# Kernel optimization log

Measured on AMD Instinct MI355X. Metric: run time of the kernel, lower is better.

## Reference

```python
import jax, jax.numpy as jnp
import numpy as np

L, D, H, DH, W, G, FF = 2, 768, 12, 64, 256, 64, 3072  # W = one-sided window (attention_window=512)
B, S = 2, 4096
NEG = -1e9


def setup_inputs() -> dict:
    key = jax.random.key(0)
    ks = jax.random.split(key, 16)
    inp = {}
    inp['hidden_states'] = jax.random.normal(ks[0], (B, S, D), jnp.float32)
    # HF Longformer convention: <0 masked, >0 global, 0 local. First G tokens are global.
    inp['attention_mask'] = jnp.zeros((B, S), jnp.float32).at[:, :G].set(1.0)
    inp['padding_len'] = 0
    inp['level_hierarchy'] = 0
    def w(k, shape):
        return (jax.random.normal(k, shape, jnp.float32) * 0.02)
    for i, n in enumerate(['Wq', 'Wk', 'Wv', 'Wqg', 'Wkg', 'Wvg', 'Wo']):
        inp[n] = w(ks[1 + i], (L, D, D))
        inp['b' + n[1:].lower()] = jnp.zeros((L, D), jnp.float32)
    inp['Wi'] = w(ks[8], (L, D, FF)); inp['bi'] = jnp.zeros((L, FF), jnp.float32)
    inp['Wo2'] = w(ks[9], (L, FF, D)); inp['bo2'] = jnp.zeros((L, D), jnp.float32)
    for n in ['ln1', 'ln2']:
        inp[n + '_g'] = jnp.ones((L, D), jnp.float32)
        inp[n + '_b'] = jnp.zeros((L, D), jnp.float32)
    return inp


def _ln(x, g, b):
    mu = jnp.mean(x, -1, keepdims=True)
    var = jnp.mean(jnp.square(x - mu), -1, keepdims=True)
    return (x - mu) * jax.lax.rsqrt(var + 1e-5) * g + b


def _chunk3(x, nc, w):
    # x: [..., S, d] -> [..., nc, 3w, d]: keys of chunks (c-1, c, c+1), zero-padded at the ends
    shp = x.shape
    xr = x.reshape(shp[:-2] + (nc, w, shp[-1]))
    pad = [(0, 0)] * xr.ndim
    pad[-3] = (1, 1)
    xp = jnp.pad(xr, pad)
    return jnp.concatenate([xp[..., :-2, :, :], xp[..., 1:-1, :, :], xp[..., 2:, :, :]], axis=-2)


def _layer(h, mask, Wq, bq, Wk, bk, Wv, bv, Wqg, bqg, Wkg, bkg, Wvg, bvg,
           Wo, bo, ln1_g, ln1_b, Wi, bi, Wo2, bo2, ln2_g, ln2_b):
    Bb, Ss, Dd = h.shape
    nc = Ss // W
    scale = 1.0 / np.sqrt(DH)
    def heads(x):
        return x.reshape(Bb, Ss, H, DH).transpose(0, 2, 1, 3)  # [B,H,S,dh]
    q = heads(h @ Wq + bq) * scale
    k = heads(h @ Wk + bk)
    v = heads(h @ Wv + bv)
    # --- sliding-window (banded) attention, chunked ---
    qc = q.reshape(Bb, H, nc, W, DH)
    k3 = _chunk3(k, nc, W)  # [B,H,nc,3W,dh]
    v3 = _chunk3(v, nc, W)
    local = jnp.einsum('bhcid,bhcjd->bhcij', qc, k3)  # [B,H,nc,W,3W]
    i = jnp.arange(W)[:, None]
    j = jnp.arange(3 * W)[None, :]
    band_ok = jnp.abs(j - W - i) <= W                              # [W,3W]
    keypos = jnp.arange(nc)[:, None, None] * W + (j - W)[None]     # [nc,1,3W]
    in_range = (keypos >= 0) & (keypos < Ss)
    # masked and global keys are removed from the windowed attention (handled via global cols)
    key_local = _chunk3((mask == 0).astype(h.dtype)[..., None], nc, W)[..., 0] > 0.5  # [B,nc,3W]
    valid = band_ok[None, None] & in_range[None] & key_local[:, :, None, :]  # [B,nc,W,3W]
    local = jnp.where(valid[:, None], local, NEG)
    # --- global key columns (every token attends to the G global tokens) ---
    kg, vg = k[:, :, :G], v[:, :, :G]
    sg = jnp.einsum('bhsd,bhgd->bhsg', q, kg).reshape(Bb, H, nc, W, G)
    probs = jax.nn.softmax(jnp.concatenate([sg, local], axis=-1), axis=-1)
    pg, pl = probs[..., :G], probs[..., G:]
    out = (jnp.einsum('bhcig,bhgd->bhcid', pg, vg)
           + jnp.einsum('bhcij,bhcjd->bhcid', pl, v3)).reshape(Bb, H, Ss, DH)
    # --- global token rows: full attention with dedicated global projections ---
    qg = heads(h @ Wqg + bqg)[:, :, :G] * scale
    kgf = heads(h @ Wkg + bkg)
    vgf = heads(h @ Wvg + bvg)
    add = jnp.where(mask < 0, NEG, 0.0)[:, None, None, :]
    pgl = jax.nn.softmax(jnp.einsum('bhgd,bhsd->bhgs', qg, kgf) + add, axis=-1)
    out = out.at[:, :, :G].set(jnp.einsum('bhgs,bhsd->bhgd', pgl, vgf))
    out = jnp.where((mask < 0)[:, None, :, None], 0.0, out)
    attn = out.transpose(0, 2, 1, 3).reshape(Bb, Ss, Dd) @ Wo + bo
    h = _ln(attn + h, ln1_g, ln1_b)
    ff = jax.nn.gelu(h @ Wi + bi, approximate=False) @ Wo2 + bo2
    return _ln(ff + h, ln2_g, ln2_b)


def reference(hidden_states, attention_mask, padding_len, level_hierarchy,
              Wq, bq, Wk, bk, Wv, bv, Wqg, bqg, Wkg, bkg, Wvg, bvg,
              Wo, bo, ln1_g, ln1_b, Wi, bi, Wo2, bo2, ln2_g, ln2_b):
    h = hidden_states
    for l in range(L):
        h = _layer(h, attention_mask,
                   Wq[l], bq[l], Wk[l], bk[l], Wv[l], bv[l],
                   Wqg[l], bqg[l], Wkg[l], bkg[l], Wvg[l], bvg[l],
                   Wo[l], bo[l], ln1_g[l], ln1_b[l],
                   Wi[l], bi[l], Wo2[l], bo2[l], ln2_g[l], ln2_b[l])
    if padding_len > 0:
        h = h[:, :-padding_len]
    return h
```

## Files before the change

### kernel.cpp

```cpp
#include <hip/hip_runtime.h>

#define B_ 2
#define S_ 4096
#define D_ 768
#define H_ 12
#define DH_ 64
#define W_ 256
#define G_ 64
#define FF_ 3072
#define L_ 2
#define M_ (B_*S_)
#define NEGV -1e9f
#define NSPLIT 16

typedef short bf16x8 __attribute__((ext_vector_type(8)));
typedef float f32x4 __attribute__((ext_vector_type(4)));
typedef unsigned short u16;
typedef unsigned short u16x4 __attribute__((ext_vector_type(4)));

__device__ __forceinline__ u16 f2bf(float f) {
  union { float f; unsigned u; } a; a.f = f;
  unsigned r = a.u + 0x7FFFu + ((a.u >> 16) & 1u);
  return (u16)(r >> 16);
}
__device__ __forceinline__ float b2f(u16 u) {
  union { unsigned u; float f; } a; a.u = ((unsigned)u) << 16;
  return a.f;
}

__device__ __forceinline__ f32x4 mfma16(bf16x8 a, bf16x8 b, f32x4 c) {
  return __builtin_amdgcn_mfma_f32_16x16x32_bf16(a, b, c, 0, 0, 0);
}

__device__ __forceinline__ void gload16(const u16* g, u16* l) {
  __builtin_amdgcn_global_load_lds((const __attribute__((address_space(1))) void*)g,
                                   (__attribute__((address_space(3))) void*)l, 16, 0, 0);
}

__device__ __forceinline__ int xcd_swz(int bid, int nwg) {
  if ((nwg & 7) == 0) {
    int cpx = nwg >> 3;
    bid = (bid & 7) * cpx + (bid >> 3);
  }
  return bid;
}

struct Ptr7 { const float* p[7]; };
__global__ __launch_bounds__(256) void wtrans7(Ptr7 in, u16* __restrict__ out) {
  __shared__ float tile[32][33];
  int z = blockIdx.z;
  int slab = z >> 1, l = z & 1;
  const float* src = in.p[slab] + (size_t)l * D_ * D_;
  u16* dst = out + (size_t)z * D_ * D_;
  int k0 = blockIdx.y * 32, n0 = blockIdx.x * 32;
  int tx = threadIdx.x, ty = threadIdx.y;
#pragma unroll
  for (int i = 0; i < 4; i++)
    tile[ty + i*8][tx] = src[(size_t)(k0 + ty + i*8) * D_ + n0 + tx];
  __syncthreads();
#pragma unroll
  for (int i = 0; i < 4; i++)
    dst[(size_t)(n0 + ty + i*8) * D_ + k0 + tx] = f2bf(tile[tx][ty + i*8]);
}

__global__ __launch_bounds__(256) void wtrans(const float* __restrict__ in,
                                              u16* __restrict__ out, int K, int N) {
  __shared__ float tile[32][33];
  size_t base = (size_t)blockIdx.z * K * N;
  int k0 = blockIdx.y * 32, n0 = blockIdx.x * 32;
  int tx = threadIdx.x, ty = threadIdx.y;
#pragma unroll
  for (int i = 0; i < 4; i++)
    tile[ty + i*8][tx] = in[base + (size_t)(k0 + ty + i*8) * N + n0 + tx];
  __syncthreads();
#pragma unroll
  for (int i = 0; i < 4; i++)
    out[base + (size_t)(n0 + ty + i*8) * K + k0 + tx] = f2bf(tile[tx][ty + i*8]);
}

__global__ __launch_bounds__(256) void conv_b(const float* __restrict__ in,
                                              u16* __restrict__ outb, int n4) {
  int i = blockIdx.x * 256 + threadIdx.x;
  if (i >= n4) return;
  float4 v = ((const float4*)in)[i];
  u16x4 o;
  o[0] = f2bf(v.x); o[1] = f2bf(v.y); o[2] = f2bf(v.z); o[3] = f2bf(v.w);
  ((u16x4*)outb)[i] = o;
}

template <int MODE>
__device__ __forceinline__ float epi_post(float v) {
  if (MODE == 2) return v * 0.125f;
  if (MODE == 3) {
    float y = 0.79788456f * (v + 0.044715f * v * v * v);
    float e = __expf(fminf(2.f * y, 20.f));
    return v * e / (e + 1.f);
  }
  return v;
}

struct Bias5 { const float* p[5]; };

#define VMC4() asm volatile("s_waitcnt vmcnt(4)" ::: "memory")
#define VMC0() asm volatile("s_waitcnt vmcnt(0)" ::: "memory")
#define GPH_PRE() do { __builtin_amdgcn_s_barrier(); \
  asm volatile("s_waitcnt lgkmcnt(0)" ::: "memory"); \
  __builtin_amdgcn_sched_barrier(0); } while (0)
#define GPH_PRE_NOLDS() do { __builtin_amdgcn_s_barrier(); \
  __builtin_amdgcn_sched_barrier(0); } while (0)
#define GPH_POST() do { __builtin_amdgcn_sched_barrier(0); \
  __builtin_amdgcn_s_barrier(); } while (0)
#define GPH_MFMA(AF, BF, QM, QN) do { \
  __builtin_amdgcn_s_setprio(1); \
  _Pragma("unroll") for (int mi = 0; mi < 4; mi++) \
  _Pragma("unroll") for (int nj = 0; nj < 2; nj++) \
  _Pragma("unroll") for (int ks = 0; ks < 2; ks++) \
    acc[(QM)*4+mi][(QN)*2+nj] = mfma16(AF[mi][ks], BF[nj][ks], acc[(QM)*4+mi][(QN)*2+nj]); \
  __builtin_amdgcn_s_setprio(0); } while (0)

template <int MODE, int NW>
__global__ __launch_bounds__(512, 2) void gemm256p(const u16* __restrict__ A,
                                                   const u16* __restrict__ Wbase,
                                                   Bias5 bp,
                                                   u16* __restrict__ OutBase,
                                                   int Kdim, int Nstride, int l) {
  __shared__ u16 sh[65536];
  int gx = gridDim.x;
  int bid = blockIdx.x + blockIdx.y * gx;
  bid = xcd_swz(bid, gx * gridDim.y);
  int bxx = bid % gx, by = bid / gx;
  int bm = by * 256;
  int widx, bn;
  const u16* Bt; u16* Cb; const float* bias;
  if (NW == 5) {
    widx = bxx / 3;
    bn = (bxx % 3) * 256;
    int slab = widx + (widx >= 3 ? 1 : 0);
    Bt = Wbase + ((size_t)slab * L_ + l) * (size_t)D_ * D_;
    Cb = OutBase + (size_t)slab * M_ * D_;
    bias = bp.p[widx];
  } else {
    widx = 0;
    bn = bxx * 256;
    Bt = Wbase; Cb = OutBase; bias = bp.p[0];
  }
  int tid = threadIdx.x;
  int lane = tid & 63, wid = tid >> 6;
  int wr = wid >> 2, wc = wid & 3;
  int lr = lane & 15, lg = lane >> 4;

  int rr0 = tid >> 3, slot0 = tid & 7;
  int c80 = slot0 ^ (rr0 & 7);
  const u16* pA = A + (size_t)(bm + rr0) * Kdim + c80 * 8;
  const u16* pB = Bt + (size_t)(bn + rr0) * Kdim + c80 * 8;

  auto stA = [&](int buf, int h, int kt) {
    u16* base = sh + buf * 16384;
    gload16(pA + (size_t)(h * 128) * Kdim + kt * 64, &base[(h * 1024 + tid) * 8]);
    gload16(pA + (size_t)(h * 128 + 64) * Kdim + kt * 64, &base[(h * 1024 + 512 + tid) * 8]);
  };
  auto stB = [&](int buf, int h, int kt) {
    u16* base = sh + 32768 + buf * 16384;
    gload16(pB + (size_t)(h * 128) * Kdim + kt * 64, &base[(h * 1024 + tid) * 8]);
    gload16(pB + (size_t)(h * 128 + 64) * Kdim + kt * 64, &base[(h * 1024 + 512 + tid) * 8]);
  };
  auto ldA = [&](bf16x8 (&af)[4][2], int c, int qm) {
    const u16* base = sh + c * 16384;
#pragma unroll
    for (int mi = 0; mi < 4; mi++)
#pragma unroll
      for (int ks = 0; ks < 2; ks++) {
        int row = wr * 128 + qm * 64 + mi * 16 + lr;
        int c8 = ks * 4 + lg;
        af[mi][ks] = *(const bf16x8*)&base[(row * 8 + (c8 ^ (row & 7))) * 8];
      }
  };
  auto ldB = [&](bf16x8 (&bf)[2][2], int c, int qn) {
    const u16* base = sh + 32768 + c * 16384;
#pragma unroll
    for (int nj = 0; nj < 2; nj++)
#pragma unroll
      for (int ks = 0; ks < 2; ks++) {
        int row = wc * 64 + qn * 32 + nj * 16 + lr;
        int c8 = ks * 4 + lg;
        bf[nj][ks] = *(const bf16x8*)&base[(row * 8 + (c8 ^ (row & 7))) * 8];
      }
  };

  f32x4 acc[8][4] = {};
  int nt = Kdim >> 6;

  stA(0, 0, 0); stA(0, 1, 0);
  stB(0, 0, 0); stB(0, 1, 0);
  stB(1, 0, 1); stB(1, 1, 1);
  VMC4();
  __builtin_amdgcn_s_barrier();

  bf16x8 af[4][2], b0[2][2], b1[2][2];
  for (int kt = 0; kt < nt; kt += 2) {
    bool notlast = (kt + 2 < nt);
    ldA(af, 0, 0); ldB(b0, 0, 0);
    stA(1, 0, kt + 1);
    GPH_PRE(); GPH_MFMA(af, b0, 0, 0); GPH_POST();
    ldB(b1, 0, 1);
    stA(1, 1, kt + 1);
    GPH_PRE(); GPH_MFMA(af, b1, 0, 1); GPH_POST();
    ldA(af, 0, 1);
    if (notlast) stB(0, 0, kt + 2);
    GPH_PRE(); GPH_MFMA(af, b0, 1, 0); GPH_POST();
    if (notlast) { stB(0, 1, kt + 2); VMC4(); } else { VMC0(); }
    GPH_PRE_NOLDS(); GPH_MFMA(af, b1, 1, 1); GPH_POST();
    ldA(af, 1, 0); ldB(b0, 1, 0);
    if (notlast) stA(0, 0, kt + 2);
    GPH_PRE(); GPH_MFMA(af, b0, 0, 0); GPH_POST();
    ldB(b1, 1, 1);
    if (notlast) stA(0, 1, kt + 2);
    GPH_PRE(); GPH_MFMA(af, b1, 0, 1); GPH_POST();
    ldA(af, 1, 1);
    if (notlast) stB(1, 0, kt + 3);
    GPH_PRE(); GPH_MFMA(af, b0, 1, 0); GPH_POST();
    if (notlast) { stB(1, 1, kt + 3); VMC4(); } else { VMC0(); }
    GPH_PRE_NOLDS(); GPH_MFMA(af, b1, 1, 1); GPH_POST();
  }

  int cr = (lane >> 4) * 4, cc = lane & 15;
  float scale = (NW == 5 && widx == 0) ? 0.125f : 1.0f;
#pragma unroll
  for (int nj = 0; nj < 4; nj++) {
    int col = wc * 64 + nj * 16 + cc;
    float bv = bias[bn + col];
#pragma unroll
    for (int mi = 0; mi < 8; mi++)
#pragma unroll
      for (int r = 0; r < 4; r++) {
        int row = wr * 128 + mi * 16 + cr + r;
        int chunk = (col >> 3) ^ (row & 31);
        sh[row * 256 + chunk * 8 + (col & 7)] =
            f2bf(epi_post<MODE>((acc[mi][nj][r] + bv) * scale));
      }
  }
  __syncthreads();
  {
    int row = tid >> 1, half = tid & 1;
    u16* gro = Cb + (size_t)(bm + row) * Nstride + bn + half * 128;
#pragma unroll
    for (int c = 0; c < 16; c++) {
      int lc = half * 16 + c;
      int pc = lc ^ (row & 31);
      bf16x8 v = *(const bf16x8*)&sh[row * 256 + pc * 8];
      *(bf16x8*)(gro + c * 8) = v;
    }
  }
}

template <int MODE>
__global__ __launch_bounds__(256) void gemm_pipe(const u16* __restrict__ A,
                                                 const u16* __restrict__ Bt,
                                                 const float* __restrict__ bias,
                                                 u16* __restrict__ Cb,
                                                 int Ndim, int Kdim, int rowTileStride) {
  __shared__ u16 sh[24576];
  int gx = gridDim.x;
  int bid = blockIdx.x + blockIdx.y * gx;
  bid = xcd_swz(bid, gx * gridDim.y);
  int bm = (bid / gx) * rowTileStride * 128;
  int bn = (bid % gx) * 128;
  int tid = threadIdx.x;
  int lane = tid & 63, w = tid >> 6;
  int r0w = (w >> 1) * 64, c0w = (w & 1) * 64;
  int lr = lane & 15, lg = lane >> 4;

  int f0 = tid, l0 = f0 >> 3, s0 = (f0 & 7) ^ (l0 & 7);
  int row0 = (l0 << 1) | (s0 >> 2), c0s = (s0 & 3) * 8;
  int f1 = tid + 256, l1 = f1 >> 3, s1 = (f1 & 7) ^ (l1 & 7);
  int row1 = (l1 << 1) | (s1 >> 2), c1s = (s1 & 3) * 8;
  const u16* A0 = A + (size_t)(bm + row0) * Kdim + c0s;
  const u16* A1 = A + (size_t)(bm + row1) * Kdim + c1s;
  const u16* B0 = Bt + (size_t)(bn + row0) * Kdim + c0s;
  const u16* B1 = Bt + (size_t)(bn + row1) * Kdim + c1s;

  int offa[4], offb[4];
#pragma unroll
  for (int i = 0; i < 4; i++) {
    int ra = r0w + i * 16 + lr;
    int la = ra >> 1, sa = ((ra & 1) << 2) | lg;
    offa[i] = la * 64 + (sa ^ (la & 7)) * 8;
    int rb = c0w + i * 16 + lr;
    int lb = rb >> 1, sb = ((rb & 1) << 2) | lg;
    offb[i] = lb * 64 + (sb ^ (lb & 7)) * 8;
  }

  auto stage = [&](int kt, int buf) {
    int k1 = kt << 5;
    u16* ab = sh + buf * 4096;
    u16* bb = sh + 12288 + buf * 4096;
    gload16(A0 + k1, &ab[tid * 8]);
    gload16(A1 + k1, &ab[tid * 8 + 2048]);
    gload16(B0 + k1, &bb[tid * 8]);
    gload16(B1 + k1, &bb[tid * 8 + 2048]);
  };

  int nt = Kdim >> 5;
  f32x4 acc[4][4] = {};

  stage(0, 0);
  if (nt > 1) stage(1, 1);

  for (int t = 0; t < nt; t++) {
    int cb = t % 3;
    if (t + 2 < nt) {
      stage(t + 2, (t + 2) % 3);
      asm volatile("s_waitcnt vmcnt(8)" ::: "memory");
    } else if (t + 1 < nt) {
      asm volatile("s_waitcnt vmcnt(4)" ::: "memory");
    } else {
      asm volatile("s_waitcnt vmcnt(0)" ::: "memory");
    }
    __builtin_amdgcn_s_barrier();
    __builtin_amdgcn_sched_barrier(0);
    const u16* ab = sh + cb * 4096;
    const u16* bb = sh + 12288 + cb * 4096;
    bf16x8 a[4], b[4];
#pragma unroll
    for (int i = 0; i < 4; i++) a[i] = *(const bf16x8*)&ab[offa[i]];
#pragma unroll
    for (int j = 0; j < 4; j++) b[j] = *(const bf16x8*)&bb[offb[j]];
#pragma unroll
    for (int i = 0; i < 4; i++)
#pragma unroll
      for (int j = 0; j < 4; j++)
        acc[i][j] = mfma16(a[i], b[j], acc[i][j]);
    __builtin_amdgcn_sched_barrier(0);
    __builtin_amdgcn_s_barrier();
    __builtin_amdgcn_sched_barrier(0);
  }

  int cr = (lane >> 4) * 4, cc = lane & 15;
#pragma unroll
  for (int j = 0; j < 4; j++) {
    int col = c0w + j * 16 + cc;
    float bv = bias[bn + col];
#pragma unroll
    for (int i = 0; i < 4; i++)
#pragma unroll
      for (int r = 0; r < 4; r++) {
        int row = r0w + i * 16 + cr + r;
        int chunk = (col >> 3) ^ (row & 15);
        sh[row * 128 + chunk * 8 + (col & 7)] =
            f2bf(epi_post<MODE>(acc[i][j][r] + bv));
      }
  }
  __syncthreads();
  {
    int row = tid >> 1, half = tid & 1;
    u16* gro = Cb + (size_t)(bm + row) * Ndim + bn + half * 64;
#pragma unroll
    for (int c = 0; c < 8; c++) {
      int lc = half * 8 + c;
      int pc = lc ^ (row & 15);
      bf16x8 v = *(const bf16x8*)&sh[row * 128 + pc * 8];
      *(bf16x8*)(gro + c * 8) = v;
    }
  }
}

__global__ __launch_bounds__(128) void attn_local(const u16* __restrict__ qb,
                                                  const u16* __restrict__ kb_,
                                                  const u16* __restrict__ vb,
                                                  const float* __restrict__ mask,
                                                  u16* __restrict__ ao) {
  int bid = blockIdx.x + blockIdx.y * gridDim.x;
  bid = xcd_swz(bid, 1536);
  int cx = bid & 63, bh = bid >> 6;
  int c = cx >> 2, sub = cx & 3;
  int b = bh / H_, h = bh % H_;
  int tid = threadIdx.x;
  int w = tid >> 6, lane = tid & 63;
  int lr = lane & 15, lg = lane >> 4;

  __shared__ u16 vtT[64][72];
  __shared__ u16 plds[2][32][72];
  __shared__ unsigned char vflag[576];

  int base_off = sub * 64;
  int kwin0 = c * W_ - W_;
  for (int i = tid; i < 576; i += 128) {
    int kp = kwin0 + base_off + i;
    vflag[i] = (kp >= 0 && kp < S_ && mask[b * S_ + kp] == 0.0f) ? 1 : 0;
  }

  size_t hoff = (size_t)b * S_ * D_ + h * DH_;
  int qrow0 = c * W_ + base_off + w * 32;
  bf16x8 aq[2][2];
#pragma unroll
  for (int fi = 0; fi < 2; fi++)
#pragma unroll
    for (int ks = 0; ks < 2; ks++)
      aq[fi][ks] = *(const bf16x8*)(qb + hoff + (size_t)(qrow0 + fi * 16 + lr) * D_ + ks * 32 + lg * 8);

  float ls[2][4];
  f32x4 o[2][4] = {};
#pragma unroll
  for (int fi = 0; fi < 2; fi++)
#pragma unroll
    for (int r = 0; r < 4; r++) ls[fi][r] = 0.f;

  int stg_k4 = tid >> 3, stg_j = tid & 7;
  int stg_dh0 = stg_j * 8;

  for (int kb = 0; kb <= 9; kb++) {
    int kstart = 0;
    if (kb > 0) {
      kstart = kwin0 + base_off + (kb - 1) * 64;
      if (kstart + 64 <= 0 || kstart >= S_) continue;
    }
    __syncthreads();
    {
#pragma unroll
      for (int p = 0; p < 4; p++) {
        int key = p * 16 + stg_k4;
        int kp = (kb ? kstart : 0) + key;
        bf16x8 row = *(const bf16x8*)(vb + hoff + (size_t)kp * D_ + stg_dh0);
        u16* basep = &vtT[stg_dh0][key ^ (stg_j << 3)];
#pragma unroll
        for (int e = 0; e < 8; e++) basep[e * 72] = (u16)row[e];
      }
    }
    __syncthreads();

    bf16x8 bk0[4], bk1[4];
#pragma unroll
    for (int nj = 0; nj < 4; nj++) {
      int kp = (kb ? kstart : 0) + nj * 16 + lr;
      const u16* ks8 = kb_ + hoff + (size_t)kp * D_ + lg * 8;
      bk0[nj] = *(const bf16x8*)(ks8);
      bk1[nj] = *(const bf16x8*)(ks8 + 32);
    }
    f32x4 sc[2][4];
#pragma unroll
    for (int fi = 0; fi < 2; fi++)
#pragma unroll
      for (int nj = 0; nj < 4; nj++) {
        f32x4 t = {};
        t = mfma16(aq[fi][0], bk0[nj], t);
        t = mfma16(aq[fi][1], bk1[nj], t);
        sc[fi][nj] = t;
      }

    if (kb >= 2 && kb <= 8) {
#pragma unroll
      for (int nj = 0; nj < 4; nj++) {
        bool kv = vflag[(kb - 1) * 64 + nj * 16 + lr] != 0;
#pragma unroll
        for (int fi = 0; fi < 2; fi++)
#pragma unroll
          for (int r = 0; r < 4; r++)
            sc[fi][nj][r] = kv ? sc[fi][nj][r] : NEGV;
      }
    } else if (kb > 0) {
#pragma unroll
      for (int nj = 0; nj < 4; nj++) {
        int fidx = (kb - 1) * 64 + nj * 16 + lr;
        int koff = base_off + fidx;
        bool kv = vflag[fidx] != 0;
#pragma unroll
        for (int fi = 0; fi < 2; fi++)
#pragma unroll
          for (int r = 0; r < 4; r++) {
            int wq = base_off + w * 32 + fi * 16 + lg * 4 + r;
            if (!(kv && koff >= wq && koff <= wq + 2 * W_)) sc[fi][nj][r] = NEGV;
          }
      }
    }

#pragma unroll
    for (int fi = 0; fi < 2; fi++)
#pragma unroll
      for (int r = 0; r < 4; r++) {
        float ps = 0.f;
#pragma unroll
        for (int nj = 0; nj < 4; nj++) {
          float p = __expf(sc[fi][nj][r]);
          sc[fi][nj][r] = p;
          ps += p;
        }
#pragma unroll
        for (int d = 1; d < 16; d <<= 1) ps += __shfl_xor(ps, d);
        ls[fi][r] += ps;
      }

#pragma unroll
    for (int fi = 0; fi < 2; fi++)
#pragma unroll
      for (int nj = 0; nj < 4; nj++)
#pragma unroll
        for (int r = 0; r < 4; r++)
          plds[w][fi * 16 + lg * 4 + r][nj * 16 + lr] = f2bf(sc[fi][nj][r]);
    asm volatile("s_waitcnt lgkmcnt(0)" ::: "memory");
    __builtin_amdgcn_sched_barrier(0);

    bf16x8 ap[2][2];
#pragma unroll
    for (int fi = 0; fi < 2; fi++)
#pragma unroll
      for (int ks = 0; ks < 2; ks++)
        ap[fi][ks] = *(const bf16x8*)&plds[w][fi * 16 + lr][ks * 32 + lg * 8];
#pragma unroll
    for (int dj = 0; dj < 4; dj++) {
      int xr = ((dj * 16 + lr) >> 3) & 7;
#pragma unroll
      for (int ks = 0; ks < 2; ks++) {
        bf16x8 bv = *(const bf16x8*)&vtT[dj * 16 + lr][(ks * 32 + lg * 8) ^ (xr << 3)];
        o[0][dj] = mfma16(ap[0][ks], bv, o[0][dj]);
        o[1][dj] = mfma16(ap[1][ks], bv, o[1][dj]);
      }
    }
  }

#pragma unroll
  for (int fi = 0; fi < 2; fi++)
#pragma unroll
    for (int dj = 0; dj < 4; dj++)
#pragma unroll
      for (int r = 0; r < 4; r++) {
        int row = qrow0 + fi * 16 + lg * 4 + r;
        float v = o[fi][dj][r] / ls[fi][r];
        ao[hoff + (size_t)row * D_ + dj * 16 + lr] = f2bf(v);
      }
}

__global__ __launch_bounds__(128) void attn_gsplit(const u16* __restrict__ qg,
                                                   const u16* __restrict__ kg,
                                                   const u16* __restrict__ vg,
                                                   float* __restrict__ opart,
                                                   float* __restrict__ lpart) {
  int sp = blockIdx.x, bh = blockIdx.y;
  int b = bh / H_, h = bh % H_;
  int tid = threadIdx.x, w = tid >> 6, lane = tid & 63;
  int lr = lane & 15, lg = lane >> 4;
  __shared__ u16 vtT[64][72];
  __shared__ u16 plds[2][32][72];
  size_t hoff = (size_t)b * S_ * D_ + h * DH_;
  int qrow0 = w * 32;
  bf16x8 aq[2][2];
#pragma unroll
  for (int fi = 0; fi < 2; fi++)
#pragma unroll
    for (int ks = 0; ks < 2; ks++)
      aq[fi][ks] = *(const bf16x8*)(qg + hoff + (size_t)(qrow0 + fi * 16 + lr) * D_ + ks * 32 + lg * 8);
  float ls[2][4];
  f32x4 o[2][4] = {};
#pragma unroll
  for (int fi = 0; fi < 2; fi++)
#pragma unroll
    for (int r = 0; r < 4; r++) ls[fi][r] = 0.f;

  int stg_k4 = tid >> 3, stg_j = tid & 7;
  int stg_dh0 = stg_j * 8;

  for (int kb = 0; kb < 4; kb++) {
    int kstart = sp * 256 + kb * 64;
    __syncthreads();
#pragma unroll
    for (int p = 0; p < 4; p++) {
      int key = p * 16 + stg_k4;
      bf16x8 row = *(const bf16x8*)(vg + hoff + (size_t)(kstart + key) * D_ + stg_dh0);
      u16* basep = &vtT[stg_dh0][key ^ (stg_j << 3)];
#pragma unroll
      for (int e = 0; e < 8; e++) basep[e * 72] = (u16)row[e];
    }
    __syncthreads();

    bf16x8 bk0[4], bk1[4];
#pragma unroll
    for (int nj = 0; nj < 4; nj++) {
      const u16* ks8 = kg + hoff + (size_t)(kstart + nj * 16 + lr) * D_ + lg * 8;
      bk0[nj] = *(const bf16x8*)(ks8);
      bk1[nj] = *(const bf16x8*)(ks8 + 32);
    }
    f32x4 sc[2][4];
#pragma unroll
    for (int fi = 0; fi < 2; fi++)
#pragma unroll
      for (int nj = 0; nj < 4; nj++) {
        f32x4 t = {};
        t = mfma16(aq[fi][0], bk0[nj], t);
        t = mfma16(aq[fi][1], bk1[nj], t);
        sc[fi][nj] = t;
      }
#pragma unroll
    for (int fi = 0; fi < 2; fi++)
#pragma unroll
      for (int r = 0; r < 4; r++) {
        float ps = 0.f;
#pragma unroll
        for (int nj = 0; nj < 4; nj++) {
          float p = __expf(sc[fi][nj][r]);
          sc[fi][nj][r] = p;
          ps += p;
        }
#pragma unroll
        for (int d = 1; d < 16; d <<= 1) ps += __shfl_xor(ps, d);
        ls[fi][r] += ps;
      }
#pragma unroll
    for (int fi = 0; fi < 2; fi++)
#pragma unroll
      for (int nj = 0; nj < 4; nj++)
#pragma unroll
        for (int r = 0; r < 4; r++)
          plds[w][fi * 16 + lg * 4 + r][nj * 16 + lr] = f2bf(sc[fi][nj][r]);
    asm volatile("s_waitcnt lgkmcnt(0)" ::: "memory");
    __builtin_amdgcn_sched_barrier(0);
    bf16x8 ap[2][2];
#pragma unroll
    for (int fi = 0; fi < 2; fi++)
#pragma unroll
      for (int ks = 0; ks < 2; ks++)
        ap[fi][ks] = *(const bf16x8*)&plds[w][fi * 16 + lr][ks * 32 + lg * 8];
#pragma unroll
    for (int dj = 0; dj < 4; dj++) {
      int xr = ((dj * 16 + lr) >> 3) & 7;
#pragma unroll
      for (int ks = 0; ks < 2; ks++) {
        bf16x8 bv = *(const bf16x8*)&vtT[dj * 16 + lr][(ks * 32 + lg * 8) ^ (xr << 3)];
        o[0][dj] = mfma16(ap[0][ks], bv, o[0][dj]);
        o[1][dj] = mfma16(ap[1][ks], bv, o[1][dj]);
      }
    }
  }

  size_t pbase = (size_t)(bh * NSPLIT + sp) * 64;
#pragma unroll
  for (int fi = 0; fi < 2; fi++)
#pragma unroll
    for (int r = 0; r < 4; r++) {
      int row = qrow0 + fi * 16 + lg * 4 + r;
      if (lr == 0) lpart[pbase + row] = ls[fi][r];
#pragma unroll
      for (int dj = 0; dj < 4; dj++)
        opart[(pbase + row) * 64 + dj * 16 + lr] = o[fi][dj][r];
    }
}

__global__ __launch_bounds__(256) void attn_gcombine(const float* __restrict__ opart,
                                                     const float* __restrict__ lpart,
                                                     u16* __restrict__ ao) {
  int bh = blockIdx.x;
  int b = bh / H_, h = bh % H_;
  int t = threadIdx.x;
  __shared__ float lt[64];
  if (t < 64) {
    float lsum = 0.f;
#pragma unroll
    for (int sp = 0; sp < NSPLIT; sp++)
      lsum += lpart[(size_t)(bh * NSPLIT + sp) * 64 + t];
    lt[t] = lsum;
  }
  __syncthreads();
  int row = t >> 2, c0 = (t & 3) * 16;
  float acc[16] = {};
  for (int sp = 0; sp < NSPLIT; sp++) {
    const float* op = opart + ((size_t)(bh * NSPLIT + sp) * 64 + row) * 64 + c0;
#pragma unroll
    for (int j = 0; j < 16; j++) acc[j] += op[j];
  }
  float inv = 1.f / lt[row];
  size_t hoff = (size_t)b * S_ * D_ + h * DH_;
#pragma unroll
  for (int j = 0; j < 16; j++)
    ao[hoff + (size_t)row * D_ + c0 + j] = f2bf(acc[j] * inv);
}

__global__ __launch_bounds__(192) void ln_b(const u16* __restrict__ x,
                                            const u16* __restrict__ res,
                                            const float* __restrict__ gg,
                                            const float* __restrict__ bb,
                                            u16* __restrict__ outb,
                                            float* __restrict__ outf) {
  int row = blockIdx.x, t = threadIdx.x;
  const u16* xr = x + (size_t)row * D_;
  const u16* rr = res + (size_t)row * D_;
  u16x4 xv = *(const u16x4*)&xr[t * 4];
  u16x4 rv = *(const u16x4*)&rr[t * 4];
  float v[4];
#pragma unroll
  for (int e = 0; e < 4; e++) v[e] = b2f(xv[e]) + b2f(rv[e]);
  __shared__ float sha[3], shb[3];
  float s = v[0] + v[1] + v[2] + v[3];
#pragma unroll
  for (int d = 1; d < 64; d <<= 1) s += __shfl_xor(s, d);
  if ((t & 63) == 0) sha[t >> 6] = s;
  __syncthreads();
  float mu = (sha[0] + sha[1] + sha[2]) * (1.f / 768.f);
  float dd[4], s2 = 0.f;
#pragma unroll
  for (int e = 0; e < 4; e++) { dd[e] = v[e] - mu; s2 += dd[e] * dd[e]; }
#pragma unroll
  for (int d = 1; d < 64; d <<= 1) s2 += __shfl_xor(s2, d);
  if ((t & 63) == 0) shb[t >> 6] = s2;
  __syncthreads();
  float var = (shb[0] + shb[1] + shb[2]) * (1.f / 768.f);
  float rs = rsqrtf(var + 1e-5f);
  float4 gv = *(const float4*)&gg[t * 4];
  float4 bv = *(const float4*)&bb[t * 4];
  float y0 = dd[0] * rs * gv.x + bv.x;
  float y1 = dd[1] * rs * gv.y + bv.y;
  float y2 = dd[2] * rs * gv.z + bv.z;
  float y3 = dd[3] * rs * gv.w + bv.w;
  u16x4 ov;
  ov[0] = f2bf(y0); ov[1] = f2bf(y1); ov[2] = f2bf(y2); ov[3] = f2bf(y3);
  *(u16x4*)&outb[(size_t)row * D_ + t * 4] = ov;
  if (outf) {
    float4 of = {y0, y1, y2, y3};
    *(float4*)&outf[(size_t)row * D_ + t * 4] = of;
  }
}

extern "C" void kernel_launch(void* const* d_in, const int* in_sizes, int n_in,
                              void* d_out, int out_size, void* d_ws, size_t ws_size,
                              hipStream_t stream) {
  (void)in_sizes; (void)n_in; (void)out_size; (void)ws_size;
  const float* hidden = (const float*)d_in[0];
  const float* mask   = (const float*)d_in[1];
  const float* Wq  = (const float*)d_in[4];   const float* bq  = (const float*)d_in[5];
  const float* Wk  = (const float*)d_in[6];   const float* bk  = (const float*)d_in[7];
  const float* Wv  = (const float*)d_in[8];   const float* bv  = (const float*)d_in[9];
  const float* Wqg = (const float*)d_in[10];  const float* bqg = (const float*)d_in[11];
  const float* Wkg = (const float*)d_in[12];  const float* bkg = (const float*)d_in[13];
  const float* Wvg = (const float*)d_in[14];  const float* bvg = (const float*)d_in[15];
  const float* Wo  = (const float*)d_in[16];  const float* bo  = (const float*)d_in[17];
  const float* Wi  = (const float*)d_in[18];  const float* bi  = (const float*)d_in[19];
  const float* Wo2 = (const float*)d_in[20];  const float* bo2 = (const float*)d_in[21];
  const float* ln1g = (const float*)d_in[22]; const float* ln1b = (const float*)d_in[23];
  const float* ln2g = (const float*)d_in[24]; const float* ln2b = (const float*)d_in[25];

  char* ws = (char*)d_ws;
  size_t off = 0;
  auto alloc = [&](size_t bytes) -> void* {
    void* p = ws + off;
    off += (bytes + 255) & ~(size_t)255;
    return p;
  };
  const size_t DD = (size_t)D_ * D_;
  const size_t DF = (size_t)D_ * FF_;
  u16* Wt = (u16*)alloc((7 * L_ * DD + 2 * L_ * DF) * 2);
  u16* wqg_t = Wt + 3 * L_ * DD;
  u16* wo_t  = Wt + 6 * L_ * DD;
  u16* wi_t  = Wt + 7 * L_ * DD;
  u16* wo2_t = Wt + 7 * L_ * DD + L_ * DF;

  u16* X0 = (u16*)alloc((size_t)M_ * D_ * 2);
  u16* X1 = (u16*)alloc((size_t)M_ * D_ * 2);
  u16* tb = (u16*)alloc((size_t)M_ * D_ * 2);
  u16* B_bf = (u16*)alloc((size_t)M_ * FF_ * 2);
  u16* qbf  = (u16*)alloc((size_t)M_ * D_ * 2);
  u16* kbf  = (u16*)alloc((size_t)M_ * D_ * 2);
  u16* vbf  = (u16*)alloc((size_t)M_ * D_ * 2);
  u16* qgbf = (u16*)alloc((size_t)M_ * D_ * 2);
  u16* kgbf = (u16*)alloc((size_t)M_ * D_ * 2);
  u16* vgbf = (u16*)alloc((size_t)M_ * D_ * 2);
  u16* aobf = (u16*)alloc((size_t)M_ * D_ * 2);
  float* opart = (float*)alloc((size_t)B_ * H_ * NSPLIT * 64 * 64 * 4);
  float* lpart = (float*)alloc((size_t)B_ * H_ * NSPLIT * 64 * 4);

  dim3 tb32(32, 8);
  Ptr7 wp;
  wp.p[0] = Wq; wp.p[1] = Wk; wp.p[2] = Wv; wp.p[3] = Wqg;
  wp.p[4] = Wkg; wp.p[5] = Wvg; wp.p[6] = Wo;
  wtrans7<<<dim3(24, 24, 14), tb32, 0, stream>>>(wp, Wt);
  wtrans<<<dim3(96, 24, 2), tb32, 0, stream>>>(Wi,  wi_t,  D_, FF_);
  wtrans<<<dim3(24, 96, 2), tb32, 0, stream>>>(Wo2, wo2_t, FF_, D_);

  conv_b<<<(M_ * D_ / 4 + 255) / 256, 256, 0, stream>>>(hidden, X0, M_ * D_ / 4);

  for (int l = 0; l < L_; l++) {
    size_t wdd = (size_t)l * DD;
    size_t wdf = (size_t)l * DF;
    dim3 g64(6, 64), g2(6, 2);

    Bias5 bp;
    bp.p[0] = bq  + l * D_;
    bp.p[1] = bk  + l * D_;
    bp.p[2] = bv  + l * D_;
    bp.p[3] = bkg + l * D_;
    bp.p[4] = bvg + l * D_;
    gemm256p<1, 5><<<dim3(15, 32), 512, 0, stream>>>(X0, Wt, bp, qbf, D_, D_, l);
    gemm_pipe<2><<<g2, 256, 0, stream>>>(X0, wqg_t + wdd, bqg + l * D_, qgbf, D_, D_, 32);

    attn_local<<<dim3((S_ / W_) * 4, B_ * H_), 128, 0, stream>>>(qbf, kbf, vbf, mask, aobf);
    attn_gsplit<<<dim3(NSPLIT, B_ * H_), 128, 0, stream>>>(qgbf, kgbf, vgbf, opart, lpart);
    attn_gcombine<<<B_ * H_, 256, 0, stream>>>(opart, lpart, aobf);

    gemm_pipe<1><<<g64, 256, 0, stream>>>(aobf, wo_t + wdd, bo + l * D_, tb, D_, D_, 1);
    ln_b<<<M_, 192, 0, stream>>>(tb, X0, ln1g + l * D_, ln1b + l * D_, X1, nullptr);

    Bias5 bpi; bpi.p[0] = bi + l * FF_;
    gemm256p<3, 1><<<dim3(12, 32), 512, 0, stream>>>(X1, wi_t + wdf, bpi, B_bf, D_, FF_, 0);
    gemm_pipe<1><<<g64, 256, 0, stream>>>(B_bf, wo2_t + wdf, bo2 + l * D_, tb, D_, FF_, 1);

    ln_b<<<M_, 192, 0, stream>>>(tb, X1, ln2g + l * D_, ln2b + l * D_, X0,
                                 (l == L_ - 1) ? (float*)d_out : nullptr);
  }
}
```

Baseline: 740.6 us.

## Widen local attention blocks to 128 queries and write GEMM epilogue directly

The local attention kernel now uses 256 threads covering 128 query rows per block, so each staged K/V key tile is shared by four waves instead of two. That halves the grid and cuts redundant K/V staging, at the cost of one extra key block per block and more shared memory. Separately, the gemm256p epilogue drops the LDS-swizzled coalesced store and writes scalar bf16 values straight to global memory. This removes a barrier and LDS traffic but produces strided, uncoalesced 2-byte stores.

```diff
diff --git a/kernel.cpp b/kernel.cpp
--- a/kernel.cpp
+++ b/kernel.cpp
@@ -223,33 +223,20 @@
     GPH_PRE_NOLDS(); GPH_MFMA(af, b1, 1, 1); GPH_POST();
   }
 
+  int r0 = bm + wr * 128, c0 = bn + wc * 64;
   int cr = (lane >> 4) * 4, cc = lane & 15;
-  float scale = (NW == 5 && widx == 0) ? 0.125f : 1.0f;
+  float sc = (NW == 5 && widx == 0) ? 0.125f : 1.0f;
 #pragma unroll
   for (int nj = 0; nj < 4; nj++) {
-    int col = wc * 64 + nj * 16 + cc;
-    float bv = bias[bn + col];
+    int col = c0 + nj * 16 + cc;
+    float bv = bias[col];
 #pragma unroll
     for (int mi = 0; mi < 8; mi++)
 #pragma unroll
       for (int r = 0; r < 4; r++) {
-        int row = wr * 128 + mi * 16 + cr + r;
-        int chunk = (col >> 3) ^ (row & 31);
-        sh[row * 256 + chunk * 8 + (col & 7)] =
-            f2bf(epi_post<MODE>((acc[mi][nj][r] + bv) * scale));
-      }
-  }
-  __syncthreads();
-  {
-    int row = tid >> 1, half = tid & 1;
-    u16* gro = Cb + (size_t)(bm + row) * Nstride + bn + half * 128;
-#pragma unroll
-    for (int c = 0; c < 16; c++) {
-      int lc = half * 16 + c;
-      int pc = lc ^ (row & 31);
-      bf16x8 v = *(const bf16x8*)&sh[row * 256 + pc * 8];
-      *(bf16x8*)(gro + c * 8) = v;
-    }
+        size_t off = (size_t)(r0 + mi * 16 + cr + r) * Nstride + col;
+        Cb[off] = f2bf(epi_post<MODE>((acc[mi][nj][r] + bv) * sc));
+      }
   }
 }
 
@@ -364,27 +351,27 @@
   }
 }
 
-__global__ __launch_bounds__(128) void attn_local(const u16* __restrict__ qb,
+__global__ __launch_bounds__(256) void attn_local(const u16* __restrict__ qb,
                                                   const u16* __restrict__ kb_,
                                                   const u16* __restrict__ vb,
                                                   const float* __restrict__ mask,
                                                   u16* __restrict__ ao) {
   int bid = blockIdx.x + blockIdx.y * gridDim.x;
-  bid = xcd_swz(bid, 1536);
-  int cx = bid & 63, bh = bid >> 6;
-  int c = cx >> 2, sub = cx & 3;
+  bid = xcd_swz(bid, 768);
+  int cx = bid & 31, bh = bid >> 5;
+  int c = cx >> 1, sub = cx & 1;
   int b = bh / H_, h = bh % H_;
   int tid = threadIdx.x;
   int w = tid >> 6, lane = tid & 63;
   int lr = lane & 15, lg = lane >> 4;
 
   __shared__ u16 vtT[64][72];
-  __shared__ u16 plds[2][32][72];
-  __shared__ unsigned char vflag[576];
-
-  int base_off = sub * 64;
+  __shared__ u16 plds[4][32][72];
+  __shared__ unsigned char vflag[640];
+
+  int base_off = sub * 128;
   int kwin0 = c * W_ - W_;
-  for (int i = tid; i < 576; i += 128) {
+  for (int i = tid; i < 640; i += 256) {
     int kp = kwin0 + base_off + i;
     vflag[i] = (kp >= 0 && kp < S_ && mask[b * S_ + kp] == 0.0f) ? 1 : 0;
   }
@@ -405,10 +392,10 @@
 #pragma unroll
     for (int r = 0; r < 4; r++) ls[fi][r] = 0.f;
 
-  int stg_k4 = tid >> 3, stg_j = tid & 7;
+  int stg_k = tid >> 3, stg_j = tid & 7;
   int stg_dh0 = stg_j * 8;
 
-  for (int kb = 0; kb <= 9; kb++) {
+  for (int kb = 0; kb <= 10; kb++) {
     int kstart = 0;
     if (kb > 0) {
       kstart = kwin0 + base_off + (kb - 1) * 64;
@@ -417,8 +404,8 @@
     __syncthreads();
     {
 #pragma unroll
-      for (int p = 0; p < 4; p++) {
-        int key = p * 16 + stg_k4;
+      for (int p = 0; p < 2; p++) {
+        int key = p * 32 + stg_k;
         int kp = (kb ? kstart : 0) + key;
         bf16x8 row = *(const bf16x8*)(vb + hoff + (size_t)kp * D_ + stg_dh0);
         u16* basep = &vtT[stg_dh0][key ^ (stg_j << 3)];
@@ -447,7 +434,7 @@
         sc[fi][nj] = t;
       }
 
-    if (kb >= 2 && kb <= 8) {
+    if (kb >= 3 && kb <= 8) {
 #pragma unroll
       for (int nj = 0; nj < 4; nj++) {
         bool kv = vflag[(kb - 1) * 64 + nj * 16 + lr] != 0;
@@ -461,14 +448,13 @@
 #pragma unroll
       for (int nj = 0; nj < 4; nj++) {
         int fidx = (kb - 1) * 64 + nj * 16 + lr;
-        int koff = base_off + fidx;
         bool kv = vflag[fidx] != 0;
 #pragma unroll
         for (int fi = 0; fi < 2; fi++)
 #pragma unroll
           for (int r = 0; r < 4; r++) {
-            int wq = base_off + w * 32 + fi * 16 + lg * 4 + r;
-            if (!(kv && koff >= wq && koff <= wq + 2 * W_)) sc[fi][nj][r] = NEGV;
+            int rq = w * 32 + fi * 16 + lg * 4 + r;
+            if (!(kv && fidx >= rq && fidx <= rq + 2 * W_)) sc[fi][nj][r] = NEGV;
           }
       }
     }
@@ -788,7 +774,7 @@
     gemm256p<1, 5><<<dim3(15, 32), 512, 0, stream>>>(X0, Wt, bp, qbf, D_, D_, l);
     gemm_pipe<2><<<g2, 256, 0, stream>>>(X0, wqg_t + wdd, bqg + l * D_, qgbf, D_, D_, 32);
 
-    attn_local<<<dim3((S_ / W_) * 4, B_ * H_), 128, 0, stream>>>(qbf, kbf, vbf, mask, aobf);
+    attn_local<<<dim3((S_ / W_) * 2, B_ * H_), 256, 0, stream>>>(qbf, kbf, vbf, mask, aobf);
     attn_gsplit<<<dim3(NSPLIT, B_ * H_), 128, 0, stream>>>(qgbf, kgbf, vgbf, opart, lpart);
     attn_gcombine<<<B_ * H_, 256, 0, stream>>>(opart, lpart, aobf);
 
```

New measurement: 704.2 us. 1.05x faster.

## Prefetch next K/V block in local attention and write GEMM epilogue directly

Applied to the files above, without the earlier changes.

The sliding-window attention loop now computes the valid key-block range up front and register-prefetches the next block's K and V while computing the current one. This hides global-load latency behind MFMA work, and raw s_barrier calls replace __syncthreads. Separately, the GEMM epilogue drops the LDS-staged coalesced store and writes bf16 outputs straight to global memory. That removes a barrier and LDS traffic but produces scattered 2-byte stores, which may hurt write coalescing.

```diff
diff --git a/kernel.cpp b/kernel.cpp
--- a/kernel.cpp
+++ b/kernel.cpp
@@ -223,33 +223,20 @@
     GPH_PRE_NOLDS(); GPH_MFMA(af, b1, 1, 1); GPH_POST();
   }
 
+  int r0 = bm + wr * 128, c0 = bn + wc * 64;
   int cr = (lane >> 4) * 4, cc = lane & 15;
-  float scale = (NW == 5 && widx == 0) ? 0.125f : 1.0f;
+  float sc = (NW == 5 && widx == 0) ? 0.125f : 1.0f;
 #pragma unroll
   for (int nj = 0; nj < 4; nj++) {
-    int col = wc * 64 + nj * 16 + cc;
-    float bv = bias[bn + col];
+    int col = c0 + nj * 16 + cc;
+    float bv = bias[col];
 #pragma unroll
     for (int mi = 0; mi < 8; mi++)
 #pragma unroll
       for (int r = 0; r < 4; r++) {
-        int row = wr * 128 + mi * 16 + cr + r;
-        int chunk = (col >> 3) ^ (row & 31);
-        sh[row * 256 + chunk * 8 + (col & 7)] =
-            f2bf(epi_post<MODE>((acc[mi][nj][r] + bv) * scale));
-      }
-  }
-  __syncthreads();
-  {
-    int row = tid >> 1, half = tid & 1;
-    u16* gro = Cb + (size_t)(bm + row) * Nstride + bn + half * 128;
-#pragma unroll
-    for (int c = 0; c < 16; c++) {
-      int lc = half * 16 + c;
-      int pc = lc ^ (row & 31);
-      bf16x8 v = *(const bf16x8*)&sh[row * 256 + pc * 8];
-      *(bf16x8*)(gro + c * 8) = v;
-    }
+        size_t off = (size_t)(r0 + mi * 16 + cr + r) * Nstride + col;
+        Cb[off] = f2bf(epi_post<MODE>((acc[mi][nj][r] + bv) * sc));
+      }
   }
 }
 
@@ -398,6 +385,15 @@
     for (int ks = 0; ks < 2; ks++)
       aq[fi][ks] = *(const bf16x8*)(qb + hoff + (size_t)(qrow0 + fi * 16 + lr) * D_ + ks * 32 + lg * 8);
 
+  int K0 = kwin0 + base_off;
+  int kb_lo = (K0 < 0) ? (1 + ((-K0) >> 6)) : 1;
+  int kb_hi = 9;
+  { int hi = 1 + ((S_ - 64 - K0) >> 6); if (hi < 9) kb_hi = hi; }
+  int niter = 1 + (kb_hi - kb_lo + 1);
+
+  int stg_k4 = tid >> 3, stg_j = tid & 7;
+  int stg_dh0 = stg_j * 8;
+
   float ls[2][4];
   f32x4 o[2][4] = {};
 #pragma unroll
@@ -405,45 +401,53 @@
 #pragma unroll
     for (int r = 0; r < 4; r++) ls[fi][r] = 0.f;
 
-  int stg_k4 = tid >> 3, stg_j = tid & 7;
-  int stg_dh0 = stg_j * 8;
-
-  for (int kb = 0; kb <= 9; kb++) {
-    int kstart = 0;
-    if (kb > 0) {
-      kstart = kwin0 + base_off + (kb - 1) * 64;
-      if (kstart + 64 <= 0 || kstart >= S_) continue;
-    }
-    __syncthreads();
-    {
-#pragma unroll
-      for (int p = 0; p < 4; p++) {
-        int key = p * 16 + stg_k4;
-        int kp = (kb ? kstart : 0) + key;
-        bf16x8 row = *(const bf16x8*)(vb + hoff + (size_t)kp * D_ + stg_dh0);
-        u16* basep = &vtT[stg_dh0][key ^ (stg_j << 3)];
-#pragma unroll
-        for (int e = 0; e < 8; e++) basep[e * 72] = (u16)row[e];
-      }
-    }
-    __syncthreads();
-
-    bf16x8 bk0[4], bk1[4];
-#pragma unroll
-    for (int nj = 0; nj < 4; nj++) {
-      int kp = (kb ? kstart : 0) + nj * 16 + lr;
-      const u16* ks8 = kb_ + hoff + (size_t)kp * D_ + lg * 8;
-      bk0[nj] = *(const bf16x8*)(ks8);
-      bk1[nj] = *(const bf16x8*)(ks8 + 32);
-    }
+  bf16x8 ck0[4], ck1[4], nk0[4], nk1[4], cv[4], nv[4];
+#pragma unroll
+  for (int nj = 0; nj < 4; nj++) {
+    const u16* ks8 = kb_ + hoff + (size_t)(nj * 16 + lr) * D_ + lg * 8;
+    ck0[nj] = *(const bf16x8*)(ks8);
+    ck1[nj] = *(const bf16x8*)(ks8 + 32);
+  }
+#pragma unroll
+  for (int p = 0; p < 4; p++)
+    cv[p] = *(const bf16x8*)(vb + hoff + (size_t)(p * 16 + stg_k4) * D_ + stg_dh0);
+
+  for (int it = 0; it < niter; it++) {
+    int kb = (it == 0) ? 0 : (kb_lo + it - 1);
+
+    __builtin_amdgcn_s_barrier();
+#pragma unroll
+    for (int p = 0; p < 4; p++) {
+      int key = p * 16 + stg_k4;
+      u16* basep = &vtT[stg_dh0][key ^ (stg_j << 3)];
+#pragma unroll
+      for (int e = 0; e < 8; e++) basep[e * 72] = (u16)cv[p][e];
+    }
+    if (it + 1 < niter) {
+      int kb2 = kb_lo + it;
+      int ks2 = K0 + (kb2 - 1) * 64;
+#pragma unroll
+      for (int nj = 0; nj < 4; nj++) {
+        const u16* ks8 = kb_ + hoff + (size_t)(ks2 + nj * 16 + lr) * D_ + lg * 8;
+        nk0[nj] = *(const bf16x8*)(ks8);
+        nk1[nj] = *(const bf16x8*)(ks8 + 32);
+      }
+#pragma unroll
+      for (int p = 0; p < 4; p++)
+        nv[p] = *(const bf16x8*)(vb + hoff + (size_t)(ks2 + p * 16 + stg_k4) * D_ + stg_dh0);
+    }
+    asm volatile("s_waitcnt lgkmcnt(0)" ::: "memory");
+    __builtin_amdgcn_s_barrier();
+    __builtin_amdgcn_sched_barrier(0);
+
     f32x4 sc[2][4];
 #pragma unroll
     for (int fi = 0; fi < 2; fi++)
 #pragma unroll
       for (int nj = 0; nj < 4; nj++) {
         f32x4 t = {};
-        t = mfma16(aq[fi][0], bk0[nj], t);
-        t = mfma16(aq[fi][1], bk1[nj], t);
+        t = mfma16(aq[fi][0], ck0[nj], t);
+        t = mfma16(aq[fi][1], ck1[nj], t);
         sc[fi][nj] = t;
       }
 
@@ -513,6 +517,13 @@
         bf16x8 bv = *(const bf16x8*)&vtT[dj * 16 + lr][(ks * 32 + lg * 8) ^ (xr << 3)];
         o[0][dj] = mfma16(ap[0][ks], bv, o[0][dj]);
         o[1][dj] = mfma16(ap[1][ks], bv, o[1][dj]);
+      }
+    }
+
+    if (it + 1 < niter) {
+#pragma unroll
+      for (int j = 0; j < 4; j++) {
+        ck0[j] = nk0[j]; ck1[j] = nk1[j]; cv[j] = nv[j];
       }
     }
   }
```

New measurement: 688.7 us. -7.0%, faster.
